# Optimization experiments

Measured on AMD Instinct MI355X. Metric: run time of the kernel, lower is better.

## Reference

```python
import jax, jax.numpy as jnp
import numpy as np

D_MODEL = 1024
NUM_HEADS = 16
D_K = D_MODEL // NUM_HEADS
SCALE = np.sqrt(D_K).astype(np.float32)


def setup_inputs() -> dict:
    key = jax.random.key(0)
    ks = jax.random.split(key, 11)
    B, S, D = 2, 2048, D_MODEL
    std = 1.0 / np.sqrt(D)
    inp = {
        "Q": jax.random.normal(ks[0], (B, S, D), dtype=jnp.float32),
        "K": jax.random.normal(ks[1], (B, S, D), dtype=jnp.float32),
        "V": jax.random.normal(ks[2], (B, S, D), dtype=jnp.float32),
        "Wq": jax.random.normal(ks[3], (D, D), dtype=jnp.float32) * std,
        "bq": jnp.zeros((D,), dtype=jnp.float32),
        "Wk": jax.random.normal(ks[4], (D, D), dtype=jnp.float32) * std,
        "bk": jnp.zeros((D,), dtype=jnp.float32),
        "Wv": jax.random.normal(ks[5], (D, D), dtype=jnp.float32) * std,
        "bv": jnp.zeros((D,), dtype=jnp.float32),
        "Wo": jax.random.normal(ks[6], (D, D), dtype=jnp.float32) * std,
        "bo": jnp.zeros((D,), dtype=jnp.float32),
    }
    return inp


def reference(Q, K, V, Wq, bq, Wk, bk, Wv, bv, Wo, bo):
    B, S, D = Q.shape
    H, dk = NUM_HEADS, D_K
    # Linear projections then split heads: [B, S, D] -> [B, H, S, dk]
    def proj(x, W, b):
        y = x @ W.T + b
        return y.reshape(B, -1, H, dk).transpose(0, 2, 1, 3)
    q = proj(Q, Wq, bq)
    k = proj(K, Wk, bk)
    v = proj(V, Wv, bv)
    # scores: [B, H, S, S]
    scores = jnp.einsum("bhqd,bhkd->bhqk", q, k) / SCALE
    attn = jax.nn.softmax(scores, axis=-1)
    # dropout is identity in eval mode
    context = jnp.einsum("bhqk,bhkd->bhqd", attn, v)
    context = context.transpose(0, 2, 1, 3).reshape(B, -1, D)
    output = context @ Wo.T + bo
    return output, attn
```

## Files before the change

### kernel.cpp

```cpp
#include <hip/hip_runtime.h>
#include <stdint.h>

#define BB 2
#define SS 2048
#define DD 1024
#define HH 16
#define DKK 64

typedef unsigned short u16;
typedef short short8 __attribute__((ext_vector_type(8)));
typedef float f32x4 __attribute__((ext_vector_type(4)));
typedef u16 u16x4 __attribute__((ext_vector_type(4)));

#define QSCALE 0.18033688011112042f

__device__ __forceinline__ u16 f2bf(float x){
  union { float f; uint32_t u; } v; v.f = x;
  uint32_t r = v.u + 0x7FFFu + ((v.u >> 16) & 1u);
  return (u16)(r >> 16);
}

struct ProjArgs {
  const void* A;
  const float* W;
  const float* bias;
  void* out;
  int mode;
  float oscale;
};

template<bool AF32>
__global__ __launch_bounds__(512)
void proj_kernel(ProjArgs a0, ProjArgs a1, ProjArgs a2)
{
  ProjArgs pa = (blockIdx.z == 0) ? a0 : (blockIdx.z == 1 ? a1 : a2);
  const int K = 1024;
  __shared__ __align__(16) u16 As[128*32];
  __shared__ __align__(16) u16 Bs[128*32];

  int tid = threadIdx.x;
  int wid = tid >> 6, lane = tid & 63;
  int lg = lane >> 4, lr = lane & 15;
  int tm = blockIdx.x * 128, tn = blockIdx.y * 128;
  int wr = (wid >> 2) * 64, wc = (wid & 3) * 32;

  const float* Af = (const float*)pa.A;
  const u16*   Ab = (const u16*)pa.A;
  const float* Wf = pa.W;

  f32x4 acc[4][2];
  #pragma unroll
  for (int m=0;m<4;m++)
    #pragma unroll
    for (int n=0;n<2;n++){ f32x4 z = {0.f,0.f,0.f,0.f}; acc[m][n] = z; }

  float4 raf[2], rbf[2];
  short8 rab;

  int s0 = tid,        r0 = s0 >> 3, c0 = (s0 & 7) * 4;
  int s1 = 512 + tid,  r1 = s1 >> 3, c1 = (s1 & 7) * 4;
  int rb_ = tid >> 2,  cb_ = (tid & 3) * 8;

  #define LOAD_TILE(kt)                                                        \
    do {                                                                       \
      if (AF32){                                                               \
        raf[0] = *(const float4*)(Af + (size_t)(tm + r0)*K + (kt) + c0);       \
        raf[1] = *(const float4*)(Af + (size_t)(tm + r1)*K + (kt) + c1);       \
      } else {                                                                 \
        rab = *(const short8*)(Ab + (size_t)(tm + rb_)*K + (kt) + cb_);        \
      }                                                                        \
      rbf[0] = *(const float4*)(Wf + (size_t)(tn + r0)*K + (kt) + c0);         \
      rbf[1] = *(const float4*)(Wf + (size_t)(tn + r1)*K + (kt) + c1);         \
    } while (0)

  LOAD_TILE(0);

  for (int kt = 0; kt < K; kt += 32){
    __syncthreads();
    if (AF32){
      u16x4 h0, h1;
      h0[0]=f2bf(raf[0].x); h0[1]=f2bf(raf[0].y); h0[2]=f2bf(raf[0].z); h0[3]=f2bf(raf[0].w);
      h1[0]=f2bf(raf[1].x); h1[1]=f2bf(raf[1].y); h1[2]=f2bf(raf[1].z); h1[3]=f2bf(raf[1].w);
      *(u16x4*)(As + r0*32 + c0) = h0;
      *(u16x4*)(As + r1*32 + c1) = h1;
    } else {
      *(short8*)(As + rb_*32 + cb_) = rab;
    }
    {
      u16x4 h0, h1;
      h0[0]=f2bf(rbf[0].x); h0[1]=f2bf(rbf[0].y); h0[2]=f2bf(rbf[0].z); h0[3]=f2bf(rbf[0].w);
      h1[0]=f2bf(rbf[1].x); h1[1]=f2bf(rbf[1].y); h1[2]=f2bf(rbf[1].z); h1[3]=f2bf(rbf[1].w);
      *(u16x4*)(Bs + r0*32 + c0) = h0;
      *(u16x4*)(Bs + r1*32 + c1) = h1;
    }
    __syncthreads();
    if (kt + 32 < K) LOAD_TILE(kt + 32);

    short8 af[4], bf[2];
    #pragma unroll
    for (int m=0;m<4;m++) af[m] = *(const short8*)(As + (wr + m*16 + lr)*32 + lg*8);
    #pragma unroll
    for (int n=0;n<2;n++) bf[n] = *(const short8*)(Bs + (wc + n*16 + lr)*32 + lg*8);
    #pragma unroll
    for (int m=0;m<4;m++)
      #pragma unroll
      for (int n=0;n<2;n++)
        acc[m][n] = __builtin_amdgcn_mfma_f32_16x16x32_bf16(af[m], bf[n], acc[m][n], 0,0,0);
  }
  #undef LOAD_TILE

  #pragma unroll
  for (int m=0;m<4;m++){
    #pragma unroll
    for (int n=0;n<2;n++){
      #pragma unroll
      for (int r=0;r<4;r++){
        int gm = tm + wr + m*16 + lg*4 + r;
        int gn = tn + wc + n*16 + lr;
        float v = (acc[m][n][r] + pa.bias[gn]) * pa.oscale;
        if (pa.mode == 3){
          __builtin_nontemporal_store(v, (float*)pa.out + (size_t)gm*DD + gn);
        } else {
          int b_ = gm >> 11, s_ = gm & 2047;
          int h_ = gn >> 6,  d_ = gn & 63;
          int bh = b_*HH + h_;
          u16 hv = f2bf(v);
          if (pa.mode == 0){
            ((u16*)pa.out)[((size_t)bh*SS + s_)*DKK + d_] = hv;
          } else if (pa.mode == 1){
            int c   = s_ >> 5;
            int lr2 = s_ & 15;
            int tl  = (s_ >> 4) & 1;
            int sub = tl*2 + (d_ >> 5);
            int lg2 = (d_ >> 3) & 3;
            int e   = d_ & 7;
            ((u16*)pa.out)[(((size_t)bh*64 + c)*4 + sub)*512 + (lg2*16 + lr2)*8 + e] = hv;
          } else {
            int c   = s_ >> 5;
            int lg2 = (s_ >> 3) & 3;
            int e   = s_ & 7;
            int dt  = d_ >> 4;
            int lr2 = d_ & 15;
            ((u16*)pa.out)[(((size_t)bh*64 + c)*4 + dt)*512 + (lg2*16 + lr2)*8 + e] = hv;
          }
        }
      }
    }
  }
}

__global__ __launch_bounds__(256, 3)
void attn_fused_kernel(const u16* __restrict__ qb, const u16* __restrict__ kf,
                       const u16* __restrict__ vf, float* __restrict__ attn_out,
                       u16* __restrict__ ctx)
{
  __shared__ __align__(16) u16 ptile[4][1280];
  __shared__ f32x4 accbuf[2][64][8];
  __shared__ float rsbuf[4][32];

  int tid = threadIdx.x;
  int w = tid >> 6, lane = tid & 63;
  int lg = lane >> 4, lr = lane & 15;
  int p = w >> 1, par = w & 1;
  int L  = blockIdx.x;
  int bh = (L & 7)*4 + ((L >> 3) & 3);
  int qg = ((L >> 5) << 1) + p;

  const u16* qp = qb + ((size_t)bh*SS + qg*32)*DKK;
  const u16* kp = kf + (size_t)bh*131072;
  const u16* vp = vf + (size_t)bh*131072;
  u16* myt = ptile[w];

  short8 qf[2][2];
  #pragma unroll
  for (int rt=0;rt<2;rt++){
    qf[rt][0] = *(const short8*)(qp + (rt*16+lr)*DKK + lg*8);
    qf[rt][1] = *(const short8*)(qp + (rt*16+lr)*DKK + 32 + lg*8);
  }

  f32x4 acc[2][4];
  #pragma unroll
  for (int rt=0;rt<2;rt++)
    #pragma unroll
    for (int dt=0;dt<4;dt++){ f32x4 z={0.f,0.f,0.f,0.f}; acc[rt][dt]=z; }
  float rsum[2] = {0.f, 0.f};

  short8 kc[4];
  #pragma unroll
  for (int s=0;s<4;s++)
    kc[s] = *(const short8*)(kp + ((size_t)par*4 + s)*512 + lane*8);

  for (int i=0;i<32;i++){
    int c = par + 2*i;
    short8 vc0 = *(const short8*)(vp + ((size_t)c*4 + 0)*512 + lane*8);
    short8 vc1 = *(const short8*)(vp + ((size_t)c*4 + 1)*512 + lane*8);
    short8 ka0=kc[0], ka1=kc[1], kb0=kc[2], kb1=kc[3];
    if (i < 31){
      #pragma unroll
      for (int s=0;s<4;s++)
        kc[s] = *(const short8*)(kp + ((size_t)(c+2)*4 + s)*512 + lane*8);
    }
    #pragma unroll
    for (int rt=0;rt<2;rt++){
      f32x4 sA = {0.f,0.f,0.f,0.f}, sB = {0.f,0.f,0.f,0.f};
      sA = __builtin_amdgcn_mfma_f32_16x16x32_bf16(ka0, qf[rt][0], sA, 0,0,0);
      sA = __builtin_amdgcn_mfma_f32_16x16x32_bf16(ka1, qf[rt][1], sA, 0,0,0);
      sB = __builtin_amdgcn_mfma_f32_16x16x32_bf16(kb0, qf[rt][0], sB, 0,0,0);
      sB = __builtin_amdgcn_mfma_f32_16x16x32_bf16(kb1, qf[rt][1], sB, 0,0,0);
      u16x4 hA, hB;
      #pragma unroll
      for (int r=0;r<4;r++){
        float pA = __builtin_exp2f(sA[r]);
        float pB = __builtin_exp2f(sB[r]);
        rsum[rt] += pA + pB;
        hA[r] = f2bf(pA);
        hB[r] = f2bf(pB);
      }
      *(u16x4*)(myt + (rt*16+lr)*40 + lg*4)      = hA;
      *(u16x4*)(myt + (rt*16+lr)*40 + 16 + lg*4) = hB;
    }
    short8 vc2 = *(const short8*)(vp + ((size_t)c*4 + 2)*512 + lane*8);
    short8 vc3 = *(const short8*)(vp + ((size_t)c*4 + 3)*512 + lane*8);
    #pragma unroll
    for (int rt=0;rt<2;rt++){
      short8 pa = *(const short8*)(myt + (rt*16+lr)*40 + lg*8);
      acc[rt][0] = __builtin_amdgcn_mfma_f32_16x16x32_bf16(pa, vc0, acc[rt][0], 0,0,0);
      acc[rt][1] = __builtin_amdgcn_mfma_f32_16x16x32_bf16(pa, vc1, acc[rt][1], 0,0,0);
      acc[rt][2] = __builtin_amdgcn_mfma_f32_16x16x32_bf16(pa, vc2, acc[rt][2], 0,0,0);
      acc[rt][3] = __builtin_amdgcn_mfma_f32_16x16x32_bf16(pa, vc3, acc[rt][3], 0,0,0);
    }
  }

  #pragma unroll
  for (int rt=0;rt<2;rt++){
    float v = rsum[rt];
    v += __shfl_xor(v, 16);
    v += __shfl_xor(v, 32);
    if (lg == 0) rsbuf[w][rt*16 + lr] = v;
  }
  if (par == 1){
    #pragma unroll
    for (int rt=0;rt<2;rt++)
      #pragma unroll
      for (int dt=0;dt<4;dt++)
        accbuf[p][lane][rt*4+dt] = acc[rt][dt];
  }
  __syncthreads();

  float il[2];
  #pragma unroll
  for (int rt=0;rt<2;rt++)
    il[rt] = 1.0f / (rsbuf[p*2][rt*16 + lr] + rsbuf[p*2+1][rt*16 + lr]);

  if (par == 0){
    int b_ = bh >> 4, h_ = bh & 15;
    #pragma unroll
    for (int rt=0;rt<2;rt++){
      #pragma unroll
      for (int dt=0;dt<4;dt++)
        acc[rt][dt] += accbuf[p][lane][rt*4+dt];
      #pragma unroll
      for (int r=0;r<4;r++){
        float ilr = __shfl(il[rt], lg*4 + r, 16);
        int row = qg*32 + rt*16 + lg*4 + r;
        #pragma unroll
        for (int dt=0;dt<4;dt++){
          float vv = acc[rt][dt][r] * ilr;
          ctx[((size_t)b_*SS + row)*DD + h_*DKK + dt*16 + lr] = f2bf(vv);
        }
      }
    }
  }

  int rt2 = par;
  float myil = il[rt2];
  short8 q0 = qf[rt2][0], q1 = qf[rt2][1];
  #pragma unroll
  for (int s=0;s<4;s++)
    kc[s] = *(const short8*)(kp + (size_t)s*512 + lane*8);
  float* arow = attn_out + ((size_t)bh*SS + qg*32 + rt2*16 + lr)*SS;
  for (int c=0;c<64;c++){
    short8 ka0=kc[0], ka1=kc[1], kb0=kc[2], kb1=kc[3];
    if (c < 63){
      #pragma unroll
      for (int s=0;s<4;s++)
        kc[s] = *(const short8*)(kp + ((size_t)(c+1)*4 + s)*512 + lane*8);
    }
    f32x4 sA = {0.f,0.f,0.f,0.f}, sB = {0.f,0.f,0.f,0.f};
    sA = __builtin_amdgcn_mfma_f32_16x16x32_bf16(ka0, q0, sA, 0,0,0);
    sA = __builtin_amdgcn_mfma_f32_16x16x32_bf16(ka1, q1, sA, 0,0,0);
    sB = __builtin_amdgcn_mfma_f32_16x16x32_bf16(kb0, q0, sB, 0,0,0);
    sB = __builtin_amdgcn_mfma_f32_16x16x32_bf16(kb1, q1, sB, 0,0,0);
    f32x4 oA, oB;
    #pragma unroll
    for (int r=0;r<4;r++){
      oA[r] = __builtin_exp2f(sA[r]) * myil;
      oB[r] = __builtin_exp2f(sB[r]) * myil;
    }
    __builtin_nontemporal_store(oA, (f32x4*)(arow + c*32 + lg*4));
    __builtin_nontemporal_store(oB, (f32x4*)(arow + c*32 + 16 + lg*4));
  }
}

extern "C" void kernel_launch(void* const* d_in, const int* in_sizes, int n_in,
                              void* d_out, int out_size, void* d_ws, size_t ws_size,
                              hipStream_t stream)
{
  const float* Q   = (const float*)d_in[0];
  const float* Kin = (const float*)d_in[1];
  const float* V   = (const float*)d_in[2];
  const float* Wq  = (const float*)d_in[3];
  const float* bq  = (const float*)d_in[4];
  const float* Wk  = (const float*)d_in[5];
  const float* bk  = (const float*)d_in[6];
  const float* Wv  = (const float*)d_in[7];
  const float* bv  = (const float*)d_in[8];
  const float* Wo  = (const float*)d_in[9];
  const float* bo  = (const float*)d_in[10];

  char* ws = (char*)d_ws;
  u16* qh  = (u16*)(ws + (size_t)( 0u<<20));
  u16* kfb = (u16*)(ws + (size_t)( 8u<<20));
  u16* vfb = (u16*)(ws + (size_t)(16u<<20));
  u16* ctx = (u16*)(ws + (size_t)(24u<<20));

  float* out0     = (float*)d_out;
  float* attn_out = out0 + (size_t)BB*SS*DD;

  ProjArgs pq = { Q,   Wq, bq, qh,   0, QSCALE };
  ProjArgs pk = { Kin, Wk, bk, kfb,  1, 1.0f   };
  ProjArgs pv = { V,   Wv, bv, vfb,  2, 1.0f   };
  ProjArgs po = { ctx, Wo, bo, out0, 3, 1.0f   };

  proj_kernel<true><<<dim3(32,8,3), 512, 0, stream>>>(pq, pk, pv);
  attn_fused_kernel<<<dim3(1024), 256, 0, stream>>>(qh, kfb, vfb, attn_out, ctx);
  proj_kernel<false><<<dim3(32,8,1), 512, 0, stream>>>(po, po, po);
}
```

Measured before the change: 299.4 us.

## Move attention-probability write into a combined epilogue kernel alongside output projection

The attention kernel now stores only the context and the per-row inverse softmax sums, leaving out the full probability matrix. A new epilogue kernel runs the output projection GEMM in 256 blocks. Its other 512 blocks recompute QK^T, apply exp2 and the stored inverse sums, and write the large attn output. The aim is to overlap the bandwidth-bound attn store with the compute-bound output projection and to lighten the attention kernel. The cost is recomputing the scores and writing a small extra workspace buffer.

```diff
diff --git a/kernel.cpp b/kernel.cpp
--- a/kernel.cpp
+++ b/kernel.cpp
@@ -150,9 +150,9 @@
 }
 
 __global__ __launch_bounds__(256, 3)
-void attn_fused_kernel(const u16* __restrict__ qb, const u16* __restrict__ kf,
-                       const u16* __restrict__ vf, float* __restrict__ attn_out,
-                       u16* __restrict__ ctx)
+void attn_ctx_kernel(const u16* __restrict__ qb, const u16* __restrict__ kf,
+                     const u16* __restrict__ vf, float* __restrict__ invl,
+                     u16* __restrict__ ctx)
 {
   __shared__ __align__(16) u16 ptile[4][1280];
   __shared__ f32x4 accbuf[2][64][8];
@@ -253,6 +253,10 @@
     il[rt] = 1.0f / (rsbuf[p*2][rt*16 + lr] + rsbuf[p*2+1][rt*16 + lr]);
 
   if (par == 0){
+    if (lg == 0){
+      invl[bh*SS + qg*32 + lr]      = il[0];
+      invl[bh*SS + qg*32 + 16 + lr] = il[1];
+    }
     int b_ = bh >> 4, h_ = bh & 15;
     #pragma unroll
     for (int rt=0;rt<2;rt++){
@@ -271,34 +275,125 @@
       }
     }
   }
-
-  int rt2 = par;
-  float myil = il[rt2];
-  short8 q0 = qf[rt2][0], q1 = qf[rt2][1];
-  #pragma unroll
-  for (int s=0;s<4;s++)
-    kc[s] = *(const short8*)(kp + (size_t)s*512 + lane*8);
-  float* arow = attn_out + ((size_t)bh*SS + qg*32 + rt2*16 + lr)*SS;
-  for (int c=0;c<64;c++){
-    short8 ka0=kc[0], ka1=kc[1], kb0=kc[2], kb1=kc[3];
-    if (c < 63){
-      #pragma unroll
-      for (int s=0;s<4;s++)
-        kc[s] = *(const short8*)(kp + ((size_t)(c+1)*4 + s)*512 + lane*8);
-    }
-    f32x4 sA = {0.f,0.f,0.f,0.f}, sB = {0.f,0.f,0.f,0.f};
-    sA = __builtin_amdgcn_mfma_f32_16x16x32_bf16(ka0, q0, sA, 0,0,0);
-    sA = __builtin_amdgcn_mfma_f32_16x16x32_bf16(ka1, q1, sA, 0,0,0);
-    sB = __builtin_amdgcn_mfma_f32_16x16x32_bf16(kb0, q0, sB, 0,0,0);
-    sB = __builtin_amdgcn_mfma_f32_16x16x32_bf16(kb1, q1, sB, 0,0,0);
-    f32x4 oA, oB;
-    #pragma unroll
-    for (int r=0;r<4;r++){
-      oA[r] = __builtin_exp2f(sA[r]) * myil;
-      oB[r] = __builtin_exp2f(sB[r]) * myil;
-    }
-    __builtin_nontemporal_store(oA, (f32x4*)(arow + c*32 + lg*4));
-    __builtin_nontemporal_store(oB, (f32x4*)(arow + c*32 + 16 + lg*4));
+}
+
+__global__ __launch_bounds__(512)
+void epilogue_kernel(const u16* __restrict__ ctxA, const float* __restrict__ Wo,
+                     const float* __restrict__ bo, float* __restrict__ out0,
+                     const u16* __restrict__ qb, const u16* __restrict__ kf,
+                     const float* __restrict__ invl, float* __restrict__ attn_out)
+{
+  __shared__ __align__(16) u16 As[128*32];
+  __shared__ __align__(16) u16 Bs[128*32];
+
+  int gb  = blockIdx.x;
+  int tid = threadIdx.x;
+  int w = tid >> 6, lane = tid & 63;
+  int lg = lane >> 4, lr = lane & 15;
+
+  if (gb >= 256){
+    int L  = gb - 256;
+    int bh = (L & 7)*4 + ((L >> 3) & 3);
+    int qrow = (L >> 5)*128 + w*16;
+    const u16* qp = qb + ((size_t)bh*SS + qrow)*DKK;
+    const u16* kp = kf + (size_t)bh*131072;
+    short8 q0 = *(const short8*)(qp + lr*DKK + lg*8);
+    short8 q1 = *(const short8*)(qp + lr*DKK + 32 + lg*8);
+    float il = invl[bh*SS + qrow + lr];
+    float* arow = attn_out + ((size_t)bh*SS + qrow + lr)*SS;
+
+    short8 kc[4];
+    #pragma unroll
+    for (int s=0;s<4;s++)
+      kc[s] = *(const short8*)(kp + (size_t)s*512 + lane*8);
+
+    for (int c=0;c<64;c++){
+      short8 ka0=kc[0], ka1=kc[1], kb0=kc[2], kb1=kc[3];
+      if (c < 63){
+        #pragma unroll
+        for (int s=0;s<4;s++)
+          kc[s] = *(const short8*)(kp + ((size_t)(c+1)*4 + s)*512 + lane*8);
+      }
+      f32x4 sA = {0.f,0.f,0.f,0.f}, sB = {0.f,0.f,0.f,0.f};
+      sA = __builtin_amdgcn_mfma_f32_16x16x32_bf16(ka0, q0, sA, 0,0,0);
+      sA = __builtin_amdgcn_mfma_f32_16x16x32_bf16(ka1, q1, sA, 0,0,0);
+      sB = __builtin_amdgcn_mfma_f32_16x16x32_bf16(kb0, q0, sB, 0,0,0);
+      sB = __builtin_amdgcn_mfma_f32_16x16x32_bf16(kb1, q1, sB, 0,0,0);
+      f32x4 oA, oB;
+      #pragma unroll
+      for (int r=0;r<4;r++){
+        oA[r] = __builtin_exp2f(sA[r]) * il;
+        oB[r] = __builtin_exp2f(sB[r]) * il;
+      }
+      __builtin_nontemporal_store(oA, (f32x4*)(arow + c*32 + lg*4));
+      __builtin_nontemporal_store(oB, (f32x4*)(arow + c*32 + 16 + lg*4));
+    }
+    return;
+  }
+
+  const int K = 1024;
+  int tm = (gb & 31) * 128, tn = (gb >> 5) * 128;
+  int wr = (w >> 2) * 64, wc = (w & 3) * 32;
+
+  f32x4 acc[4][2];
+  #pragma unroll
+  for (int m=0;m<4;m++)
+    #pragma unroll
+    for (int n=0;n<2;n++){ f32x4 z = {0.f,0.f,0.f,0.f}; acc[m][n] = z; }
+
+  float4 rbf[2];
+  short8 rab;
+  int s0 = tid,        r0 = s0 >> 3, c0 = (s0 & 7) * 4;
+  int s1 = 512 + tid,  r1 = s1 >> 3, c1 = (s1 & 7) * 4;
+  int rb_ = tid >> 2,  cb_ = (tid & 3) * 8;
+
+  #define LOAD_TILE2(kt)                                                       \
+    do {                                                                       \
+      rab    = *(const short8*)(ctxA + (size_t)(tm + rb_)*K + (kt) + cb_);     \
+      rbf[0] = *(const float4*)(Wo + (size_t)(tn + r0)*K + (kt) + c0);         \
+      rbf[1] = *(const float4*)(Wo + (size_t)(tn + r1)*K + (kt) + c1);         \
+    } while (0)
+
+  LOAD_TILE2(0);
+
+  for (int kt = 0; kt < K; kt += 32){
+    __syncthreads();
+    *(short8*)(As + rb_*32 + cb_) = rab;
+    {
+      u16x4 h0, h1;
+      h0[0]=f2bf(rbf[0].x); h0[1]=f2bf(rbf[0].y); h0[2]=f2bf(rbf[0].z); h0[3]=f2bf(rbf[0].w);
+      h1[0]=f2bf(rbf[1].x); h1[1]=f2bf(rbf[1].y); h1[2]=f2bf(rbf[1].z); h1[3]=f2bf(rbf[1].w);
+      *(u16x4*)(Bs + r0*32 + c0) = h0;
+      *(u16x4*)(Bs + r1*32 + c1) = h1;
+    }
+    __syncthreads();
+    if (kt + 32 < K) LOAD_TILE2(kt + 32);
+
+    short8 af[4], bf[2];
+    #pragma unroll
+    for (int m=0;m<4;m++) af[m] = *(const short8*)(As + (wr + m*16 + lr)*32 + lg*8);
+    #pragma unroll
+    for (int n=0;n<2;n++) bf[n] = *(const short8*)(Bs + (wc + n*16 + lr)*32 + lg*8);
+    #pragma unroll
+    for (int m=0;m<4;m++)
+      #pragma unroll
+      for (int n=0;n<2;n++)
+        acc[m][n] = __builtin_amdgcn_mfma_f32_16x16x32_bf16(af[m], bf[n], acc[m][n], 0,0,0);
+  }
+  #undef LOAD_TILE2
+
+  #pragma unroll
+  for (int m=0;m<4;m++){
+    #pragma unroll
+    for (int n=0;n<2;n++){
+      #pragma unroll
+      for (int r=0;r<4;r++){
+        int gm = tm + wr + m*16 + lg*4 + r;
+        int gn = tn + wc + n*16 + lr;
+        float v = acc[m][n][r] + bo[gn];
+        __builtin_nontemporal_store(v, out0 + (size_t)gm*DD + gn);
+      }
+    }
   }
 }
 
@@ -319,10 +414,11 @@
   const float* bo  = (const float*)d_in[10];
 
   char* ws = (char*)d_ws;
-  u16* qh  = (u16*)(ws + (size_t)( 0u<<20));
-  u16* kfb = (u16*)(ws + (size_t)( 8u<<20));
-  u16* vfb = (u16*)(ws + (size_t)(16u<<20));
-  u16* ctx = (u16*)(ws + (size_t)(24u<<20));
+  u16*   qh   = (u16*)(ws + (size_t)( 0u<<20));
+  u16*   kfb  = (u16*)(ws + (size_t)( 8u<<20));
+  u16*   vfb  = (u16*)(ws + (size_t)(16u<<20));
+  u16*   ctx  = (u16*)(ws + (size_t)(24u<<20));
+  float* invl = (float*)(ws + (size_t)(32u<<20));
 
   float* out0     = (float*)d_out;
   float* attn_out = out0 + (size_t)BB*SS*DD;
@@ -330,9 +426,9 @@
   ProjArgs pq = { Q,   Wq, bq, qh,   0, QSCALE };
   ProjArgs pk = { Kin, Wk, bk, kfb,  1, 1.0f   };
   ProjArgs pv = { V,   Wv, bv, vfb,  2, 1.0f   };
-  ProjArgs po = { ctx, Wo, bo, out0, 3, 1.0f   };
 
   proj_kernel<true><<<dim3(32,8,3), 512, 0, stream>>>(pq, pk, pv);
-  attn_fused_kernel<<<dim3(1024), 256, 0, stream>>>(qh, kfb, vfb, attn_out, ctx);
-  proj_kernel<false><<<dim3(32,8,1), 512, 0, stream>>>(po, po, po);
+  attn_ctx_kernel<<<dim3(1024), 256, 0, stream>>>(qh, kfb, vfb, invl, ctx);
+  epilogue_kernel<<<dim3(768), 512, 0, stream>>>(ctx, Wo, bo, out0,
+                                                 qh, kfb, invl, attn_out);
 }
```

Result: slower. 351.2 us (+17.3%).

## Fuse output projection into attention kernel with atomic-counter dependency tracking

Applied to the files above, without the earlier changes.

Merges the output projection into the attention launch. The extra 256 blocks each compute a 128x128 output tile once the attention blocks that write its ctx rows have signalled completion through per-tile atomic counters. This removes one kernel launch and lets the output GEMM overlap with the attention probability writeback. The cost is a memset per call, spin-waiting blocks that may occupy CU slots, and reliance on the block scheduling order to avoid deadlock.

```diff
diff --git a/kernel.cpp b/kernel.cpp
--- a/kernel.cpp
+++ b/kernel.cpp
@@ -29,7 +29,6 @@
   float oscale;
 };
 
-template<bool AF32>
 __global__ __launch_bounds__(512)
 void proj_kernel(ProjArgs a0, ProjArgs a1, ProjArgs a2)
 {
@@ -45,7 +44,6 @@
   int wr = (wid >> 2) * 64, wc = (wid & 3) * 32;
 
   const float* Af = (const float*)pa.A;
-  const u16*   Ab = (const u16*)pa.A;
   const float* Wf = pa.W;
 
   f32x4 acc[4][2];
@@ -55,20 +53,13 @@
     for (int n=0;n<2;n++){ f32x4 z = {0.f,0.f,0.f,0.f}; acc[m][n] = z; }
 
   float4 raf[2], rbf[2];
-  short8 rab;
-
   int s0 = tid,        r0 = s0 >> 3, c0 = (s0 & 7) * 4;
   int s1 = 512 + tid,  r1 = s1 >> 3, c1 = (s1 & 7) * 4;
-  int rb_ = tid >> 2,  cb_ = (tid & 3) * 8;
 
   #define LOAD_TILE(kt)                                                        \
     do {                                                                       \
-      if (AF32){                                                               \
-        raf[0] = *(const float4*)(Af + (size_t)(tm + r0)*K + (kt) + c0);       \
-        raf[1] = *(const float4*)(Af + (size_t)(tm + r1)*K + (kt) + c1);       \
-      } else {                                                                 \
-        rab = *(const short8*)(Ab + (size_t)(tm + rb_)*K + (kt) + cb_);        \
-      }                                                                        \
+      raf[0] = *(const float4*)(Af + (size_t)(tm + r0)*K + (kt) + c0);         \
+      raf[1] = *(const float4*)(Af + (size_t)(tm + r1)*K + (kt) + c1);         \
       rbf[0] = *(const float4*)(Wf + (size_t)(tn + r0)*K + (kt) + c0);         \
       rbf[1] = *(const float4*)(Wf + (size_t)(tn + r1)*K + (kt) + c1);         \
     } while (0)
@@ -77,21 +68,17 @@
 
   for (int kt = 0; kt < K; kt += 32){
     __syncthreads();
-    if (AF32){
+    {
       u16x4 h0, h1;
       h0[0]=f2bf(raf[0].x); h0[1]=f2bf(raf[0].y); h0[2]=f2bf(raf[0].z); h0[3]=f2bf(raf[0].w);
       h1[0]=f2bf(raf[1].x); h1[1]=f2bf(raf[1].y); h1[2]=f2bf(raf[1].z); h1[3]=f2bf(raf[1].w);
       *(u16x4*)(As + r0*32 + c0) = h0;
       *(u16x4*)(As + r1*32 + c1) = h1;
-    } else {
-      *(short8*)(As + rb_*32 + cb_) = rab;
-    }
-    {
-      u16x4 h0, h1;
-      h0[0]=f2bf(rbf[0].x); h0[1]=f2bf(rbf[0].y); h0[2]=f2bf(rbf[0].z); h0[3]=f2bf(rbf[0].w);
-      h1[0]=f2bf(rbf[1].x); h1[1]=f2bf(rbf[1].y); h1[2]=f2bf(rbf[1].z); h1[3]=f2bf(rbf[1].w);
-      *(u16x4*)(Bs + r0*32 + c0) = h0;
-      *(u16x4*)(Bs + r1*32 + c1) = h1;
+      u16x4 g0, g1;
+      g0[0]=f2bf(rbf[0].x); g0[1]=f2bf(rbf[0].y); g0[2]=f2bf(rbf[0].z); g0[3]=f2bf(rbf[0].w);
+      g1[0]=f2bf(rbf[1].x); g1[1]=f2bf(rbf[1].y); g1[2]=f2bf(rbf[1].z); g1[3]=f2bf(rbf[1].w);
+      *(u16x4*)(Bs + r0*32 + c0) = g0;
+      *(u16x4*)(Bs + r1*32 + c1) = g1;
     }
     __syncthreads();
     if (kt + 32 < K) LOAD_TILE(kt + 32);
@@ -118,31 +105,27 @@
         int gm = tm + wr + m*16 + lg*4 + r;
         int gn = tn + wc + n*16 + lr;
         float v = (acc[m][n][r] + pa.bias[gn]) * pa.oscale;
-        if (pa.mode == 3){
-          __builtin_nontemporal_store(v, (float*)pa.out + (size_t)gm*DD + gn);
+        int b_ = gm >> 11, s_ = gm & 2047;
+        int h_ = gn >> 6,  d_ = gn & 63;
+        int bh = b_*HH + h_;
+        u16 hv = f2bf(v);
+        if (pa.mode == 0){
+          ((u16*)pa.out)[((size_t)bh*SS + s_)*DKK + d_] = hv;
+        } else if (pa.mode == 1){
+          int c   = s_ >> 5;
+          int lr2 = s_ & 15;
+          int tl  = (s_ >> 4) & 1;
+          int sub = tl*2 + (d_ >> 5);
+          int lg2 = (d_ >> 3) & 3;
+          int e   = d_ & 7;
+          ((u16*)pa.out)[(((size_t)bh*64 + c)*4 + sub)*512 + (lg2*16 + lr2)*8 + e] = hv;
         } else {
-          int b_ = gm >> 11, s_ = gm & 2047;
-          int h_ = gn >> 6,  d_ = gn & 63;
-          int bh = b_*HH + h_;
-          u16 hv = f2bf(v);
-          if (pa.mode == 0){
-            ((u16*)pa.out)[((size_t)bh*SS + s_)*DKK + d_] = hv;
-          } else if (pa.mode == 1){
-            int c   = s_ >> 5;
-            int lr2 = s_ & 15;
-            int tl  = (s_ >> 4) & 1;
-            int sub = tl*2 + (d_ >> 5);
-            int lg2 = (d_ >> 3) & 3;
-            int e   = d_ & 7;
-            ((u16*)pa.out)[(((size_t)bh*64 + c)*4 + sub)*512 + (lg2*16 + lr2)*8 + e] = hv;
-          } else {
-            int c   = s_ >> 5;
-            int lg2 = (s_ >> 3) & 3;
-            int e   = s_ & 7;
-            int dt  = d_ >> 4;
-            int lr2 = d_ & 15;
-            ((u16*)pa.out)[(((size_t)bh*64 + c)*4 + dt)*512 + (lg2*16 + lr2)*8 + e] = hv;
-          }
+          int c   = s_ >> 5;
+          int lg2 = (s_ >> 3) & 3;
+          int e   = s_ & 7;
+          int dt  = d_ >> 4;
+          int lr2 = d_ & 15;
+          ((u16*)pa.out)[(((size_t)bh*64 + c)*4 + dt)*512 + (lg2*16 + lr2)*8 + e] = hv;
         }
       }
     }
@@ -150,155 +133,246 @@
 }
 
 __global__ __launch_bounds__(256, 3)
-void attn_fused_kernel(const u16* __restrict__ qb, const u16* __restrict__ kf,
-                       const u16* __restrict__ vf, float* __restrict__ attn_out,
-                       u16* __restrict__ ctx)
+void attn_out_kernel(const u16* __restrict__ qb, const u16* __restrict__ kf,
+                     const u16* __restrict__ vf, float* __restrict__ attn_out,
+                     u16* __restrict__ ctx, const float* __restrict__ Wo,
+                     const float* __restrict__ bo, float* __restrict__ out0,
+                     unsigned* __restrict__ ctr)
 {
-  __shared__ __align__(16) u16 ptile[4][1280];
-  __shared__ f32x4 accbuf[2][64][8];
-  __shared__ float rsbuf[4][32];
-
+  __shared__ __align__(16) char ldsbuf[27136];
   int tid = threadIdx.x;
   int w = tid >> 6, lane = tid & 63;
   int lg = lane >> 4, lr = lane & 15;
-  int p = w >> 1, par = w & 1;
-  int L  = blockIdx.x;
-  int bh = (L & 7)*4 + ((L >> 3) & 3);
-  int qg = ((L >> 5) << 1) + p;
-
-  const u16* qp = qb + ((size_t)bh*SS + qg*32)*DKK;
-  const u16* kp = kf + (size_t)bh*131072;
-  const u16* vp = vf + (size_t)bh*131072;
-  u16* myt = ptile[w];
-
-  short8 qf[2][2];
-  #pragma unroll
-  for (int rt=0;rt<2;rt++){
-    qf[rt][0] = *(const short8*)(qp + (rt*16+lr)*DKK + lg*8);
-    qf[rt][1] = *(const short8*)(qp + (rt*16+lr)*DKK + 32 + lg*8);
+  int L = blockIdx.x;
+
+  if (L < 1024){
+    u16*   ptile  = (u16*)ldsbuf;
+    f32x4* accbuf = (f32x4*)(ldsbuf + 10240);
+    float* rsbuf  = (float*)(ldsbuf + 26624);
+
+    int p = w >> 1, par = w & 1;
+    int bh = (L & 7)*4 + ((L >> 3) & 3);
+    int qg = ((L >> 5) << 1) + p;
+
+    const u16* qp = qb + ((size_t)bh*SS + qg*32)*DKK;
+    const u16* kp = kf + (size_t)bh*131072;
+    const u16* vp = vf + (size_t)bh*131072;
+    u16* myt = ptile + w*1280;
+
+    short8 qf[2][2];
+    #pragma unroll
+    for (int rt=0;rt<2;rt++){
+      qf[rt][0] = *(const short8*)(qp + (rt*16+lr)*DKK + lg*8);
+      qf[rt][1] = *(const short8*)(qp + (rt*16+lr)*DKK + 32 + lg*8);
+    }
+
+    f32x4 acc[2][4];
+    #pragma unroll
+    for (int rt=0;rt<2;rt++)
+      #pragma unroll
+      for (int dt=0;dt<4;dt++){ f32x4 z={0.f,0.f,0.f,0.f}; acc[rt][dt]=z; }
+    float rsum[2] = {0.f, 0.f};
+
+    short8 kc[4];
+    #pragma unroll
+    for (int s=0;s<4;s++)
+      kc[s] = *(const short8*)(kp + ((size_t)par*4 + s)*512 + lane*8);
+
+    for (int i=0;i<32;i++){
+      int c = par + 2*i;
+      short8 vc0 = *(const short8*)(vp + ((size_t)c*4 + 0)*512 + lane*8);
+      short8 vc1 = *(const short8*)(vp + ((size_t)c*4 + 1)*512 + lane*8);
+      short8 ka0=kc[0], ka1=kc[1], kb0=kc[2], kb1=kc[3];
+      if (i < 31){
+        #pragma unroll
+        for (int s=0;s<4;s++)
+          kc[s] = *(const short8*)(kp + ((size_t)(c+2)*4 + s)*512 + lane*8);
+      }
+      #pragma unroll
+      for (int rt=0;rt<2;rt++){
+        f32x4 sA = {0.f,0.f,0.f,0.f}, sB = {0.f,0.f,0.f,0.f};
+        sA = __builtin_amdgcn_mfma_f32_16x16x32_bf16(ka0, qf[rt][0], sA, 0,0,0);
+        sA = __builtin_amdgcn_mfma_f32_16x16x32_bf16(ka1, qf[rt][1], sA, 0,0,0);
+        sB = __builtin_amdgcn_mfma_f32_16x16x32_bf16(kb0, qf[rt][0], sB, 0,0,0);
+        sB = __builtin_amdgcn_mfma_f32_16x16x32_bf16(kb1, qf[rt][1], sB, 0,0,0);
+        u16x4 hA, hB;
+        #pragma unroll
+        for (int r=0;r<4;r++){
+          float pA = __builtin_exp2f(sA[r]);
+          float pB = __builtin_exp2f(sB[r]);
+          rsum[rt] += pA + pB;
+          hA[r] = f2bf(pA);
+          hB[r] = f2bf(pB);
+        }
+        *(u16x4*)(myt + (rt*16+lr)*40 + lg*4)      = hA;
+        *(u16x4*)(myt + (rt*16+lr)*40 + 16 + lg*4) = hB;
+      }
+      short8 vc2 = *(const short8*)(vp + ((size_t)c*4 + 2)*512 + lane*8);
+      short8 vc3 = *(const short8*)(vp + ((size_t)c*4 + 3)*512 + lane*8);
+      #pragma unroll
+      for (int rt=0;rt<2;rt++){
+        short8 pa = *(const short8*)(myt + (rt*16+lr)*40 + lg*8);
+        acc[rt][0] = __builtin_amdgcn_mfma_f32_16x16x32_bf16(pa, vc0, acc[rt][0], 0,0,0);
+        acc[rt][1] = __builtin_amdgcn_mfma_f32_16x16x32_bf16(pa, vc1, acc[rt][1], 0,0,0);
+        acc[rt][2] = __builtin_amdgcn_mfma_f32_16x16x32_bf16(pa, vc2, acc[rt][2], 0,0,0);
+        acc[rt][3] = __builtin_amdgcn_mfma_f32_16x16x32_bf16(pa, vc3, acc[rt][3], 0,0,0);
+      }
+    }
+
+    #pragma unroll
+    for (int rt=0;rt<2;rt++){
+      float v = rsum[rt];
+      v += __shfl_xor(v, 16);
+      v += __shfl_xor(v, 32);
+      if (lg == 0) rsbuf[w*32 + rt*16 + lr] = v;
+    }
+    if (par == 1){
+      #pragma unroll
+      for (int rt=0;rt<2;rt++)
+        #pragma unroll
+        for (int dt=0;dt<4;dt++)
+          accbuf[((size_t)p*64 + lane)*8 + rt*4 + dt] = acc[rt][dt];
+    }
+    __syncthreads();
+
+    float il[2];
+    #pragma unroll
+    for (int rt=0;rt<2;rt++)
+      il[rt] = 1.0f / (rsbuf[(p*2)*32 + rt*16 + lr] + rsbuf[(p*2+1)*32 + rt*16 + lr]);
+
+    if (par == 0){
+      int b_ = bh >> 4, h_ = bh & 15;
+      #pragma unroll
+      for (int rt=0;rt<2;rt++){
+        #pragma unroll
+        for (int dt=0;dt<4;dt++)
+          acc[rt][dt] += accbuf[((size_t)p*64 + lane)*8 + rt*4 + dt];
+        #pragma unroll
+        for (int r=0;r<4;r++){
+          float ilr = __shfl(il[rt], lg*4 + r, 16);
+          int row = qg*32 + rt*16 + lg*4 + r;
+          #pragma unroll
+          for (int dt=0;dt<4;dt++){
+            float vv = acc[rt][dt][r] * ilr;
+            ctx[((size_t)b_*SS + row)*DD + h_*DKK + dt*16 + lr] = f2bf(vv);
+          }
+        }
+      }
+      __threadfence();
+      if (lane == 0){
+        unsigned tix = (unsigned)((bh >> 4)*16 + (L >> 6));
+        __hip_atomic_fetch_add(&ctr[tix], 1u, __ATOMIC_RELEASE, __HIP_MEMORY_SCOPE_AGENT);
+      }
+    }
+
+    int rt2 = par;
+    float myil = il[rt2];
+    short8 q0 = qf[rt2][0], q1 = qf[rt2][1];
+    #pragma unroll
+    for (int s=0;s<4;s++)
+      kc[s] = *(const short8*)(kp + (size_t)s*512 + lane*8);
+    float* arow = attn_out + ((size_t)bh*SS + qg*32 + rt2*16 + lr)*SS;
+    for (int c=0;c<64;c++){
+      short8 ka0=kc[0], ka1=kc[1], kb0=kc[2], kb1=kc[3];
+      if (c < 63){
+        #pragma unroll
+        for (int s=0;s<4;s++)
+          kc[s] = *(const short8*)(kp + ((size_t)(c+1)*4 + s)*512 + lane*8);
+      }
+      f32x4 sA = {0.f,0.f,0.f,0.f}, sB = {0.f,0.f,0.f,0.f};
+      sA = __builtin_amdgcn_mfma_f32_16x16x32_bf16(ka0, q0, sA, 0,0,0);
+      sA = __builtin_amdgcn_mfma_f32_16x16x32_bf16(ka1, q1, sA, 0,0,0);
+      sB = __builtin_amdgcn_mfma_f32_16x16x32_bf16(kb0, q0, sB, 0,0,0);
+      sB = __builtin_amdgcn_mfma_f32_16x16x32_bf16(kb1, q1, sB, 0,0,0);
+      f32x4 oA, oB;
+      #pragma unroll
+      for (int r=0;r<4;r++){
+        oA[r] = __builtin_exp2f(sA[r]) * myil;
+        oB[r] = __builtin_exp2f(sB[r]) * myil;
+      }
+      __builtin_nontemporal_store(oA, (f32x4*)(arow + c*32 + lg*4));
+      __builtin_nontemporal_store(oB, (f32x4*)(arow + c*32 + 16 + lg*4));
+    }
+    return;
   }
 
-  f32x4 acc[2][4];
-  #pragma unroll
-  for (int rt=0;rt<2;rt++)
-    #pragma unroll
-    for (int dt=0;dt<4;dt++){ f32x4 z={0.f,0.f,0.f,0.f}; acc[rt][dt]=z; }
-  float rsum[2] = {0.f, 0.f};
-
-  short8 kc[4];
-  #pragma unroll
-  for (int s=0;s<4;s++)
-    kc[s] = *(const short8*)(kp + ((size_t)par*4 + s)*512 + lane*8);
-
-  for (int i=0;i<32;i++){
-    int c = par + 2*i;
-    short8 vc0 = *(const short8*)(vp + ((size_t)c*4 + 0)*512 + lane*8);
-    short8 vc1 = *(const short8*)(vp + ((size_t)c*4 + 1)*512 + lane*8);
-    short8 ka0=kc[0], ka1=kc[1], kb0=kc[2], kb1=kc[3];
-    if (i < 31){
-      #pragma unroll
-      for (int s=0;s<4;s++)
-        kc[s] = *(const short8*)(kp + ((size_t)(c+2)*4 + s)*512 + lane*8);
-    }
-    #pragma unroll
-    for (int rt=0;rt<2;rt++){
-      f32x4 sA = {0.f,0.f,0.f,0.f}, sB = {0.f,0.f,0.f,0.f};
-      sA = __builtin_amdgcn_mfma_f32_16x16x32_bf16(ka0, qf[rt][0], sA, 0,0,0);
-      sA = __builtin_amdgcn_mfma_f32_16x16x32_bf16(ka1, qf[rt][1], sA, 0,0,0);
-      sB = __builtin_amdgcn_mfma_f32_16x16x32_bf16(kb0, qf[rt][0], sB, 0,0,0);
-      sB = __builtin_amdgcn_mfma_f32_16x16x32_bf16(kb1, qf[rt][1], sB, 0,0,0);
-      u16x4 hA, hB;
-      #pragma unroll
-      for (int r=0;r<4;r++){
-        float pA = __builtin_exp2f(sA[r]);
-        float pB = __builtin_exp2f(sB[r]);
-        rsum[rt] += pA + pB;
-        hA[r] = f2bf(pA);
-        hB[r] = f2bf(pB);
-      }
-      *(u16x4*)(myt + (rt*16+lr)*40 + lg*4)      = hA;
-      *(u16x4*)(myt + (rt*16+lr)*40 + 16 + lg*4) = hB;
-    }
-    short8 vc2 = *(const short8*)(vp + ((size_t)c*4 + 2)*512 + lane*8);
-    short8 vc3 = *(const short8*)(vp + ((size_t)c*4 + 3)*512 + lane*8);
-    #pragma unroll
-    for (int rt=0;rt<2;rt++){
-      short8 pa = *(const short8*)(myt + (rt*16+lr)*40 + lg*8);
-      acc[rt][0] = __builtin_amdgcn_mfma_f32_16x16x32_bf16(pa, vc0, acc[rt][0], 0,0,0);
-      acc[rt][1] = __builtin_amdgcn_mfma_f32_16x16x32_bf16(pa, vc1, acc[rt][1], 0,0,0);
-      acc[rt][2] = __builtin_amdgcn_mfma_f32_16x16x32_bf16(pa, vc2, acc[rt][2], 0,0,0);
-      acc[rt][3] = __builtin_amdgcn_mfma_f32_16x16x32_bf16(pa, vc3, acc[rt][3], 0,0,0);
-    }
-  }
-
-  #pragma unroll
-  for (int rt=0;rt<2;rt++){
-    float v = rsum[rt];
-    v += __shfl_xor(v, 16);
-    v += __shfl_xor(v, 32);
-    if (lg == 0) rsbuf[w][rt*16 + lr] = v;
-  }
-  if (par == 1){
-    #pragma unroll
-    for (int rt=0;rt<2;rt++)
-      #pragma unroll
-      for (int dt=0;dt<4;dt++)
-        accbuf[p][lane][rt*4+dt] = acc[rt][dt];
-  }
-  __syncthreads();
-
-  float il[2];
-  #pragma unroll
-  for (int rt=0;rt<2;rt++)
-    il[rt] = 1.0f / (rsbuf[p*2][rt*16 + lr] + rsbuf[p*2+1][rt*16 + lr]);
-
-  if (par == 0){
-    int b_ = bh >> 4, h_ = bh & 15;
-    #pragma unroll
-    for (int rt=0;rt<2;rt++){
-      #pragma unroll
-      for (int dt=0;dt<4;dt++)
-        acc[rt][dt] += accbuf[p][lane][rt*4+dt];
-      #pragma unroll
-      for (int r=0;r<4;r++){
-        float ilr = __shfl(il[rt], lg*4 + r, 16);
-        int row = qg*32 + rt*16 + lg*4 + r;
-        #pragma unroll
-        for (int dt=0;dt<4;dt++){
-          float vv = acc[rt][dt][r] * ilr;
-          ctx[((size_t)b_*SS + row)*DD + h_*DKK + dt*16 + lr] = f2bf(vv);
+  {
+    u16* As = (u16*)ldsbuf;
+    u16* Bs = (u16*)(ldsbuf + 8192);
+    const int K = 1024;
+    int gb = L - 1024;
+    int tm = (gb & 31) * 128, tn = (gb >> 5) * 128;
+    int wr = (w >> 1) * 64, wc = (w & 1) * 64;
+
+    if (tid == 0){
+      unsigned tix = (unsigned)(tm >> 7);
+      while (__hip_atomic_load(&ctr[tix], __ATOMIC_ACQUIRE, __HIP_MEMORY_SCOPE_AGENT) < 64u)
+        __builtin_amdgcn_s_sleep(8);
+    }
+    __syncthreads();
+
+    f32x4 acc[4][4];
+    #pragma unroll
+    for (int m=0;m<4;m++)
+      #pragma unroll
+      for (int n=0;n<4;n++){ f32x4 z = {0.f,0.f,0.f,0.f}; acc[m][n] = z; }
+
+    short8 rab[2];
+    float4 rbf[4];
+    int a0 = tid,       ar0 = a0 >> 2, ac0 = (a0 & 3) * 8;
+    int a1 = 256 + tid, ar1 = a1 >> 2, ac1 = (a1 & 3) * 8;
+    int b0 = tid,       br0 = b0 >> 3, bc0 = (b0 & 7) * 4;
+
+    #define LOAD_TILE2(kt)                                                     \
+      do {                                                                     \
+        rab[0] = *(const short8*)(ctx + (size_t)(tm + ar0)*K + (kt) + ac0);    \
+        rab[1] = *(const short8*)(ctx + (size_t)(tm + ar1)*K + (kt) + ac1);    \
+        _Pragma("unroll")                                                      \
+        for (int i=0;i<4;i++)                                                  \
+          rbf[i] = *(const float4*)(Wo + (size_t)(tn + br0 + i*32)*K + (kt) + bc0); \
+      } while (0)
+
+    LOAD_TILE2(0);
+
+    for (int kt = 0; kt < K; kt += 32){
+      __syncthreads();
+      *(short8*)(As + ar0*32 + ac0) = rab[0];
+      *(short8*)(As + ar1*32 + ac1) = rab[1];
+      #pragma unroll
+      for (int i=0;i<4;i++){
+        u16x4 h;
+        h[0]=f2bf(rbf[i].x); h[1]=f2bf(rbf[i].y); h[2]=f2bf(rbf[i].z); h[3]=f2bf(rbf[i].w);
+        *(u16x4*)(Bs + (br0 + i*32)*32 + bc0) = h;
+      }
+      __syncthreads();
+      if (kt + 32 < K) LOAD_TILE2(kt + 32);
+
+      short8 af[4], bf[4];
+      #pragma unroll
+      for (int m=0;m<4;m++) af[m] = *(const short8*)(As + (wr + m*16 + lr)*32 + lg*8);
+      #pragma unroll
+      for (int n=0;n<4;n++) bf[n] = *(const short8*)(Bs + (wc + n*16 + lr)*32 + lg*8);
+      #pragma unroll
+      for (int m=0;m<4;m++)
+        #pragma unroll
+        for (int n=0;n<4;n++)
+          acc[m][n] = __builtin_amdgcn_mfma_f32_16x16x32_bf16(af[m], bf[n], acc[m][n], 0,0,0);
+    }
+    #undef LOAD_TILE2
+
+    #pragma unroll
+    for (int m=0;m<4;m++){
+      #pragma unroll
+      for (int n=0;n<4;n++){
+        #pragma unroll
+        for (int r=0;r<4;r++){
+          int gm = tm + wr + m*16 + lg*4 + r;
+          int gn = tn + wc + n*16 + lr;
+          float v = acc[m][n][r] + bo[gn];
+          __builtin_nontemporal_store(v, out0 + (size_t)gm*DD + gn);
         }
       }
     }
-  }
-
-  int rt2 = par;
-  float myil = il[rt2];
-  short8 q0 = qf[rt2][0], q1 = qf[rt2][1];
-  #pragma unroll
-  for (int s=0;s<4;s++)
-    kc[s] = *(const short8*)(kp + (size_t)s*512 + lane*8);
-  float* arow = attn_out + ((size_t)bh*SS + qg*32 + rt2*16 + lr)*SS;
-  for (int c=0;c<64;c++){
-    short8 ka0=kc[0], ka1=kc[1], kb0=kc[2], kb1=kc[3];
-    if (c < 63){
-      #pragma unroll
-      for (int s=0;s<4;s++)
-        kc[s] = *(const short8*)(kp + ((size_t)(c+1)*4 + s)*512 + lane*8);
-    }
-    f32x4 sA = {0.f,0.f,0.f,0.f}, sB = {0.f,0.f,0.f,0.f};
-    sA = __builtin_amdgcn_mfma_f32_16x16x32_bf16(ka0, q0, sA, 0,0,0);
-    sA = __builtin_amdgcn_mfma_f32_16x16x32_bf16(ka1, q1, sA, 0,0,0);
-    sB = __builtin_amdgcn_mfma_f32_16x16x32_bf16(kb0, q0, sB, 0,0,0);
-    sB = __builtin_amdgcn_mfma_f32_16x16x32_bf16(kb1, q1, sB, 0,0,0);
-    f32x4 oA, oB;
-    #pragma unroll
-    for (int r=0;r<4;r++){
-      oA[r] = __builtin_exp2f(sA[r]) * myil;
-      oB[r] = __builtin_exp2f(sB[r]) * myil;
-    }
-    __builtin_nontemporal_store(oA, (f32x4*)(arow + c*32 + lg*4));
-    __builtin_nontemporal_store(oB, (f32x4*)(arow + c*32 + 16 + lg*4));
   }
 }
 
@@ -319,10 +393,11 @@
   const float* bo  = (const float*)d_in[10];
 
   char* ws = (char*)d_ws;
-  u16* qh  = (u16*)(ws + (size_t)( 0u<<20));
-  u16* kfb = (u16*)(ws + (size_t)( 8u<<20));
-  u16* vfb = (u16*)(ws + (size_t)(16u<<20));
-  u16* ctx = (u16*)(ws + (size_t)(24u<<20));
+  u16*      qh  = (u16*)(ws + (size_t)( 0u<<20));
+  u16*      kfb = (u16*)(ws + (size_t)( 8u<<20));
+  u16*      vfb = (u16*)(ws + (size_t)(16u<<20));
+  u16*      ctx = (u16*)(ws + (size_t)(24u<<20));
+  unsigned* ctr = (unsigned*)(ws + (size_t)(33u<<20));
 
   float* out0     = (float*)d_out;
   float* attn_out = out0 + (size_t)BB*SS*DD;
@@ -330,9 +405,9 @@
   ProjArgs pq = { Q,   Wq, bq, qh,   0, QSCALE };
   ProjArgs pk = { Kin, Wk, bk, kfb,  1, 1.0f   };
   ProjArgs pv = { V,   Wv, bv, vfb,  2, 1.0f   };
-  ProjArgs po = { ctx, Wo, bo, out0, 3, 1.0f   };
-
-  proj_kernel<true><<<dim3(32,8,3), 512, 0, stream>>>(pq, pk, pv);
-  attn_fused_kernel<<<dim3(1024), 256, 0, stream>>>(qh, kfb, vfb, attn_out, ctx);
-  proj_kernel<false><<<dim3(32,8,1), 512, 0, stream>>>(po, po, po);
+
+  hipMemsetAsync(ctr, 0, 32*sizeof(unsigned), stream);
+  proj_kernel<<<dim3(32,8,3), 512, 0, stream>>>(pq, pk, pv);
+  attn_out_kernel<<<dim3(1280), 256, 0, stream>>>(qh, kfb, vfb, attn_out, ctx,
+                                                  Wo, bo, out0, ctr);
 }
```

Result: slower. 422.0 us (+40.9%).
